# Performance work log

Measured on AMD Instinct MI355X. Metric: run time of the kernel, lower is better.

The kernel has to match this reference:

```python
import jax, jax.numpy as jnp
import numpy as np

B, DIM, S = 8, 512, 1024
H, DH = 8, 64
FF_INNER = 1024      # dim * (ff_mult//2)
CONV_INNER = 1024    # dim * expansion_factor
K = 31
PAD = (K - 1) // 2


def _bn(x, g, b):
    # eval-mode BatchNorm2d with running stats (0,1) absorbed: per-channel affine
    return x * g[None, :, None, None] + b[None, :, None, None]


def _pw(x, w, b):
    # 1x1 Conv2d == channel matmul. x: [B,C,S,1], w: [O,C]
    return jnp.einsum('oc,bcst->bost', w, x) + b[None, :, None, None]


def _ff(x, g, b, w1, b1, w2, b2):
    h = _pw(_bn(x, g, b), w1, b1)
    return _pw(jax.nn.silu(h), w2, b2)


def _attn(x, g, b, wq, bq, wk, bk, wv, bv, wo, bo):
    xn = _bn(x, g, b)
    q = _pw(xn, wq, bq)[..., 0].reshape(B, H, DH, S)
    k = _pw(xn, wk, bk)[..., 0].reshape(B, H, DH, S)
    v = _pw(xn, wv, bv)[..., 0].reshape(B, H, DH, S)
    scale = DH ** -0.5
    scores = jnp.einsum('bhds,bhdt->bhst', q, k) * scale   # [B,H,S,S]
    w = jax.nn.softmax(scores, axis=-1)
    o = jnp.einsum('bhst,bhdt->bhds', w, v).reshape(B, H * DH, S)[..., None]
    return _pw(o, wo, bo)


def _conv(x, g, b, pw1_w, pw1_b, dconv_w, dconv_b, cbn_g, cbn_b, pw2_w, pw2_b):
    h = _pw(_bn(x, g, b), pw1_w, pw1_b)          # [B,2*CONV_INNER,S,1]
    a, gate = jnp.split(h, 2, axis=1)
    h = a * jax.nn.sigmoid(gate)                  # GLU
    h = jnp.transpose(h, (0, 1, 3, 2))            # [B,C,1,S] so kernel (1,K) runs along seq
    h = jax.lax.conv_general_dilated(
        h, dconv_w, window_strides=(1, 1), padding=((0, 0), (PAD, PAD)),
        dimension_numbers=('NCHW', 'OIHW', 'NCHW'))
    h = jnp.transpose(h, (0, 1, 3, 2)) + dconv_b[None, :, None, None]
    h = jax.nn.silu(_bn(h, cbn_g, cbn_b))
    return _pw(h, pw2_w, pw2_b)


def setup_inputs() -> dict:
    key = jax.random.key(0)
    ks = iter(jax.random.split(key, 32))
    w = lambda *s: jax.random.normal(next(ks), s, jnp.float32) * 0.02
    d = {
        'x': jax.random.normal(next(ks), (B, DIM, S, 1), jnp.float32),
        'ff1_g': jnp.ones((DIM,)), 'ff1_b': jnp.zeros((DIM,)),
        'ff1_w1': w(FF_INNER, DIM), 'ff1_b1': jnp.zeros((FF_INNER,)),
        'ff1_w2': w(DIM, FF_INNER), 'ff1_b2': jnp.zeros((DIM,)),
        'attn_g': jnp.ones((DIM,)), 'attn_b': jnp.zeros((DIM,)),
        'wq': w(H * DH, DIM), 'bq': jnp.zeros((H * DH,)),
        'wk': w(H * DH, DIM), 'bk': jnp.zeros((H * DH,)),
        'wv': w(H * DH, DIM), 'bv': jnp.zeros((H * DH,)),
        'wo': w(DIM, H * DH), 'bo': jnp.zeros((DIM,)),
        'conv_g': jnp.ones((DIM,)), 'conv_b': jnp.zeros((DIM,)),
        'pw1_w': w(2 * CONV_INNER, DIM), 'pw1_b': jnp.zeros((2 * CONV_INNER,)),
        'dconv_w': w(CONV_INNER, CONV_INNER, 1, K), 'dconv_b': jnp.zeros((CONV_INNER,)),
        'cbn_g': jnp.ones((CONV_INNER,)), 'cbn_b': jnp.zeros((CONV_INNER,)),
        'pw2_w': w(DIM, CONV_INNER), 'pw2_b': jnp.zeros((DIM,)),
        'ff2_g': jnp.ones((DIM,)), 'ff2_b': jnp.zeros((DIM,)),
        'ff2_w1': w(FF_INNER, DIM), 'ff2_b1': jnp.zeros((FF_INNER,)),
        'ff2_w2': w(DIM, FF_INNER), 'ff2_b2': jnp.zeros((DIM,)),
        'fin_g': jnp.ones((DIM,)), 'fin_b': jnp.zeros((DIM,)),
    }
    return d


def reference(x, ff1_g, ff1_b, ff1_w1, ff1_b1, ff1_w2, ff1_b2,
              attn_g, attn_b, wq, bq, wk, bk, wv, bv, wo, bo,
              conv_g, conv_b, pw1_w, pw1_b, dconv_w, dconv_b, cbn_g, cbn_b, pw2_w, pw2_b,
              ff2_g, ff2_b, ff2_w1, ff2_b1, ff2_w2, ff2_b2, fin_g, fin_b):
    x1 = x + 0.5 * _ff(x, ff1_g, ff1_b, ff1_w1, ff1_b1, ff1_w2, ff1_b2)
    x2 = x1 + _attn(x1, attn_g, attn_b, wq, bq, wk, bk, wv, bv, wo, bo)
    x3 = x2 + _conv(x2, conv_g, conv_b, pw1_w, pw1_b, dconv_w, dconv_b, cbn_g, cbn_b, pw2_w, pw2_b)
    x4 = x3 + 0.5 * _ff(x3, ff2_g, ff2_b, ff2_w1, ff2_b1, ff2_w2, ff2_b2)
    return _bn(x4, fin_g, fin_b)
```

## Files before the change

kernel.cpp:

```cpp
#include <hip/hip_runtime.h>
#include <cstdint>
#include <cstddef>

using bf16 = __bf16;
typedef __bf16 bf16x8 __attribute__((ext_vector_type(8)));
typedef float f32x4 __attribute__((ext_vector_type(4)));
typedef unsigned int uint4v __attribute__((ext_vector_type(4)));

#define NB 8
#define DIM 512
#define SEQ 1024
#define NH 8
#define DH 64
#define CONV_INNER 1024
#define KW 31
#define PADW 15
#define HPRA 1056

__device__ __forceinline__ float fsigmoid(float x) { return 1.f / (1.f + __expf(-x)); }
__device__ __forceinline__ float fsilu(float x) { return x * fsigmoid(x); }

__device__ __forceinline__ void gld16(const bf16* g, bf16* l) {
  __builtin_amdgcn_global_load_lds(
      (const __attribute__((address_space(1))) unsigned int*)g,
      (__attribute__((address_space(3))) unsigned int*)l, 16, 0, 0);
}


__global__ __launch_bounds__(256) void k_diag(float* __restrict__ out, int n, float v) {
  int i = blockIdx.x * 256 + threadIdx.x;
  if (i < n) out[i] = v;
}


struct CvtArgs {
  const float* s[10];
  bf16* d[10];
  int cum[11];
};

__global__ __launch_bounds__(256) void k_convert_all(CvtArgs a) {
  int blk = blockIdx.x;
  int seg = 0;
#pragma unroll
  for (int t = 0; t < 10; ++t)
    if (blk >= a.cum[t + 1]) seg = t + 1;
  const float* src = a.s[seg];
  bf16* dst = a.d[seg];
  int i = ((blk - a.cum[seg]) * 256 + threadIdx.x) * 4;
  float4 v = *reinterpret_cast<const float4*>(src + i);
  dst[i]     = (bf16)v.x;
  dst[i + 1] = (bf16)v.y;
  dst[i + 2] = (bf16)v.z;
  dst[i + 3] = (bf16)v.w;
}

__global__ __launch_bounds__(256) void k_conv_wt(const float* __restrict__ w,
                                                 bf16* __restrict__ wt) {
  __shared__ float t[256 * KW];
  int o = blockIdx.x, i0 = blockIdx.y * 256;
  const float* src = w + (size_t)o * (CONV_INNER * KW) + (size_t)i0 * KW;
  for (int idx = threadIdx.x; idx < 256 * KW; idx += 256) t[idx] = src[idx];
  __syncthreads();
  for (int k = 0; k < KW; ++k) {
    wt[((size_t)k * CONV_INNER + o) * CONV_INNER + i0 + threadIdx.x] =
        (bf16)t[threadIdx.x * KW + k];
  }
}

__global__ __launch_bounds__(256) void k_pad_zero(bf16* __restrict__ hpad) {
  int i = blockIdx.x * 256 + threadIdx.x;
  int b = i / (32 * 128);
  int r = (i >> 7) & 31;
  int c8 = (i & 127) * 8;
  int row = (r < PADW) ? r : 1024 + r;
  uint4v z = {0u, 0u, 0u, 0u};
  *reinterpret_cast<uint4v*>(&hpad[((size_t)b * HPRA + row) * CONV_INNER + c8]) = z;
}

__global__ __launch_bounds__(256) void k_transpose_in(const float* __restrict__ x,
                                                      const float* __restrict__ g,
                                                      const float* __restrict__ bvec,
                                                      float* __restrict__ xT,
                                                      bf16* __restrict__ xbn) {
  __shared__ float t[32][33];
  int s0 = blockIdx.x * 32, c0 = blockIdx.y * 32, b = blockIdx.z;
  int col = threadIdx.x & 31, rq = threadIdx.x >> 5;
#pragma unroll
  for (int i = 0; i < 4; ++i) {
    int row = rq + i * 8;
    t[row][col] = x[((size_t)b * DIM + c0 + row) * SEQ + s0 + col];
  }
  __syncthreads();
  float gg = g[c0 + col], bb = bvec[c0 + col];
#pragma unroll
  for (int i = 0; i < 4; ++i) {
    int srow = rq + i * 8;
    float v = t[col][srow];
    size_t off = ((size_t)b * SEQ + s0 + srow) * DIM + c0 + col;
    xT[off] = v;
    xbn[off] = (bf16)(v * gg + bb);
  }
}

__global__ __launch_bounds__(256) void k_concat_bias(const float* __restrict__ bq,
                                                     const float* __restrict__ bk,
                                                     const float* __restrict__ bv,
                                                     float* __restrict__ qb) {
  int i = blockIdx.x * 256 + threadIdx.x;
  if (i < 512) qb[i] = bq[i];
  else if (i < 1024) qb[i] = bk[i - 512];
  else if (i < 1536) qb[i] = bv[i - 1024];
}

template <int EPI>
__global__ __launch_bounds__(256) void k_gemm(const bf16* __restrict__ A,
                                              const bf16* __restrict__ W,
                                              const float* __restrict__ bias,
                                              const float* __restrict__ res,
                                              const float* __restrict__ g,
                                              const float* __restrict__ bb,
                                              float* __restrict__ outf,
                                              bf16* __restrict__ outb, int N, int K) {
  __shared__ __align__(16) bf16 sA[2][128 * 64];
  __shared__ __align__(16) bf16 sB[2][128 * 64];
  const int tid = threadIdx.x;
  const int b = blockIdx.z;
  const int m0 = blockIdx.y * 128, n0 = blockIdx.x * 128;
  const int lane = tid & 63, wid = tid >> 6;
  const int wm = (wid & 1) * 64, wn = (wid >> 1) * 64;
  const int fr = lane & 15, fg = lane >> 4;
  const int srow = lane >> 3;
  const int scol = ((lane & 7) ^ srow) * 8;

  f32x4 acc[4][4];
#pragma unroll
  for (int i = 0; i < 4; ++i)
#pragma unroll
    for (int j = 0; j < 4; ++j) acc[i][j] = (f32x4)0.f;

  const bf16* Abase = A + ((size_t)b * SEQ + m0 + srow) * K + scol;
  const bf16* Wbase = W + (size_t)(n0 + srow) * K + scol;
  const int nch = K >> 6;

#pragma unroll
  for (int c = 0; c < 4; ++c) {
    const int ch = wid + c * 4;
    gld16(Abase + (size_t)(ch * 8) * K, &sA[0][ch * 512]);
    gld16(Wbase + (size_t)(ch * 8) * K, &sB[0][ch * 512]);
  }
  __syncthreads();

  int buf = 0;
  for (int kt = 0; kt < nch; ++kt) {
    if (kt + 1 < nch) {
      const int kc = (kt + 1) * 64;
#pragma unroll
      for (int c = 0; c < 4; ++c) {
        const int ch = wid + c * 4;
        gld16(Abase + (size_t)(ch * 8) * K + kc, &sA[buf ^ 1][ch * 512]);
        gld16(Wbase + (size_t)(ch * 8) * K + kc, &sB[buf ^ 1][ch * 512]);
      }
    }
#pragma unroll
    for (int kk = 0; kk < 2; ++kk) {
      const int cg = kk * 4 + fg;
      bf16x8 aF[4], bF[4];
#pragma unroll
      for (int i = 0; i < 4; ++i) {
        const int ar = wm + i * 16 + fr;
        aF[i] = *reinterpret_cast<const bf16x8*>(
            &sA[buf][ar * 64 + ((cg ^ (ar & 7)) * 8)]);
        const int br = wn + i * 16 + fr;
        bF[i] = *reinterpret_cast<const bf16x8*>(
            &sB[buf][br * 64 + ((cg ^ (br & 7)) * 8)]);
      }
#pragma unroll
      for (int mi = 0; mi < 4; ++mi)
#pragma unroll
        for (int ni = 0; ni < 4; ++ni)
          acc[mi][ni] = __builtin_amdgcn_mfma_f32_16x16x32_bf16(aF[mi], bF[ni],
                                                                acc[mi][ni], 0, 0, 0);
    }
    __syncthreads();
    buf ^= 1;
  }

#pragma unroll
  for (int mi = 0; mi < 4; ++mi) {
#pragma unroll
    for (int ni = 0; ni < 4; ++ni) {
      int ncol = n0 + wn + ni * 16 + fr;
      float bv = bias[ncol];
      if constexpr (EPI == 5) {
        float gg = g[ncol], bbv = bb[ncol];
        int mrow0 = m0 + wm + mi * 16 + fg * 4;
        float v[4];
#pragma unroll
        for (int j = 0; j < 4; ++j) {
          float a = acc[mi][ni][j] + bv;
          float r = res[((size_t)b * SEQ + mrow0 + j) * 512 + ncol] + 0.5f * a;
          v[j] = r * gg + bbv;
        }
        *reinterpret_cast<float4*>(outf + ((size_t)b * 512 + ncol) * SEQ + mrow0) =
            make_float4(v[0], v[1], v[2], v[3]);
      } else {
#pragma unroll
        for (int j = 0; j < 4; ++j) {
          int mrow = m0 + wm + mi * 16 + fg * 4 + j;
          size_t off = ((size_t)b * SEQ + mrow) * N + ncol;
          float a = acc[mi][ni][j] + bv;
          if constexpr (EPI == 0) {
            outb[off] = (bf16)fsilu(a);
          } else if constexpr (EPI == 2) {
            outb[off] = (bf16)a;
          } else if constexpr (EPI == 1) {
            float r = res[off] + 0.5f * a;
            outf[off] = r;
            outb[off] = (bf16)(r * g[ncol] + bb[ncol]);
          } else if constexpr (EPI == 3) {
            float r = res[off] + a;
            outf[off] = r;
            outb[off] = (bf16)(r * g[ncol] + bb[ncol]);
          }
        }
      }
    }
  }
}

__global__ __launch_bounds__(256) void k_pw1_glu(const bf16* __restrict__ A,
                                                 const bf16* __restrict__ W,
                                                 const float* __restrict__ bias,
                                                 bf16* __restrict__ hpad) {
  __shared__ __align__(16) bf16 sA[128 * 64];
  __shared__ __align__(16) bf16 sBa[128 * 64];
  __shared__ __align__(16) bf16 sBg[128 * 64];
  const int tid = threadIdx.x;
  const int b = blockIdx.z;
  const int m0 = blockIdx.y * 128, n0 = blockIdx.x * 128;
  const int lane = tid & 63, wid = tid >> 6;
  const int wm = (wid & 1) * 64, wn = (wid >> 1) * 64;
  const int fr = lane & 15, fg = lane >> 4;
  const int srow = lane >> 3;
  const int scol = ((lane & 7) ^ srow) * 8;
  const int K = 512;

  f32x4 accA[4][4], accG[4][4];
#pragma unroll
  for (int i = 0; i < 4; ++i)
#pragma unroll
    for (int j = 0; j < 4; ++j) { accA[i][j] = (f32x4)0.f; accG[i][j] = (f32x4)0.f; }

  const bf16* Abase = A + ((size_t)b * SEQ + m0 + srow) * K + scol;
  const bf16* WaB = W + (size_t)(n0 + srow) * K + scol;
  const bf16* WgB = W + (size_t)(n0 + 1024 + srow) * K + scol;

  for (int kt = 0; kt < 8; ++kt) {
    const int kc = kt * 64;
#pragma unroll
    for (int c = 0; c < 4; ++c) {
      const int ch = wid + c * 4;
      gld16(Abase + (size_t)(ch * 8) * K + kc, &sA[ch * 512]);
      gld16(WaB + (size_t)(ch * 8) * K + kc, &sBa[ch * 512]);
      gld16(WgB + (size_t)(ch * 8) * K + kc, &sBg[ch * 512]);
    }
    __syncthreads();
#pragma unroll
    for (int kk = 0; kk < 2; ++kk) {
      const int cg = kk * 4 + fg;
      bf16x8 aF[4], bFa[4], bFg[4];
#pragma unroll
      for (int i = 0; i < 4; ++i) {
        const int ar = wm + i * 16 + fr;
        aF[i] = *reinterpret_cast<const bf16x8*>(
            &sA[ar * 64 + ((cg ^ (ar & 7)) * 8)]);
        const int br = wn + i * 16 + fr;
        bFa[i] = *reinterpret_cast<const bf16x8*>(
            &sBa[br * 64 + ((cg ^ (br & 7)) * 8)]);
        bFg[i] = *reinterpret_cast<const bf16x8*>(
            &sBg[br * 64 + ((cg ^ (br & 7)) * 8)]);
      }
#pragma unroll
      for (int mi = 0; mi < 4; ++mi)
#pragma unroll
        for (int ni = 0; ni < 4; ++ni) {
          accA[mi][ni] =
              __builtin_amdgcn_mfma_f32_16x16x32_bf16(aF[mi], bFa[ni], accA[mi][ni], 0, 0, 0);
          accG[mi][ni] =
              __builtin_amdgcn_mfma_f32_16x16x32_bf16(aF[mi], bFg[ni], accG[mi][ni], 0, 0, 0);
        }
    }
    __syncthreads();
  }

#pragma unroll
  for (int mi = 0; mi < 4; ++mi) {
#pragma unroll
    for (int ni = 0; ni < 4; ++ni) {
      int ncol = n0 + wn + ni * 16 + fr;
      float ba = bias[ncol], bg = bias[ncol + 1024];
#pragma unroll
      for (int j = 0; j < 4; ++j) {
        int mrow = m0 + wm + mi * 16 + fg * 4 + j;
        float av = accA[mi][ni][j] + ba;
        float gv = accG[mi][ni][j] + bg;
        hpad[((size_t)b * HPRA + PADW + mrow) * CONV_INNER + ncol] =
            (bf16)(av * fsigmoid(gv));
      }
    }
  }
}

__global__ __launch_bounds__(256) void k_conv(const bf16* __restrict__ hpad,
                                              const bf16* __restrict__ wt,
                                              const float* __restrict__ bias,
                                              const float* __restrict__ g,
                                              const float* __restrict__ bb,
                                              bf16* __restrict__ outb) {
  __shared__ __align__(16) bf16 sA[160 * 64];
  __shared__ __align__(16) bf16 sB0[128 * 64];
  __shared__ __align__(16) bf16 sB1[128 * 64];
  const int tid = threadIdx.x;
  const int b = blockIdx.z;
  const int n0 = blockIdx.x * 128, m0 = blockIdx.y * 128;
  const int lane = tid & 63, wid = tid >> 6;
  const int wm = (wid & 1) * 64, wn = (wid >> 1) * 64;
  const int fr = lane & 15, fg = lane >> 4;
  const int srow = lane >> 3;
  const int scol = ((lane & 7) ^ srow) * 8;

  f32x4 acc[4][4];
#pragma unroll
  for (int i = 0; i < 4; ++i)
#pragma unroll
    for (int j = 0; j < 4; ++j) acc[i][j] = (f32x4)0.f;

  const bf16* Abase = hpad + ((size_t)b * HPRA + m0 + srow) * CONV_INNER + scol;
  const bf16* Wbase = wt + (size_t)(n0 + srow) * CONV_INNER + scol;

  for (int it = 0; it < 16; ++it) {
    const int itc = it * 64;
#pragma unroll
    for (int c = 0; c < 5; ++c) {
      const int ch = wid + c * 4;
      gld16(Abase + (size_t)(ch * 8) * CONV_INNER + itc, &sA[ch * 512]);
    }
#pragma unroll
    for (int c = 0; c < 4; ++c) {
      const int ch = wid + c * 4;
      gld16(Wbase + (size_t)(ch * 8) * CONV_INNER + itc, &sB0[ch * 512]);
    }
    __syncthreads();

    for (int ks = 0; ks < KW; ++ks) {
      const bf16* cur = (ks & 1) ? sB1 : sB0;
      bf16* nxt = (ks & 1) ? sB0 : sB1;
      if (ks + 1 < KW) {
#pragma unroll
        for (int c = 0; c < 4; ++c) {
          const int ch = wid + c * 4;
          gld16(Wbase + (size_t)(ks + 1) * CONV_INNER * CONV_INNER +
                    (size_t)(ch * 8) * CONV_INNER + itc,
                &nxt[ch * 512]);
        }
      }
#pragma unroll
      for (int kk = 0; kk < 2; ++kk) {
        const int cg = kk * 4 + fg;
        bf16x8 aF[4], bF[4];
#pragma unroll
        for (int i = 0; i < 4; ++i) {
          const int ar = ks + wm + i * 16 + fr;
          aF[i] = *reinterpret_cast<const bf16x8*>(
              &sA[ar * 64 + ((cg ^ (ar & 7)) * 8)]);
        }
#pragma unroll
        for (int n = 0; n < 4; ++n) {
          const int br = wn + n * 16 + fr;
          bF[n] = *reinterpret_cast<const bf16x8*>(
              &cur[br * 64 + ((cg ^ (br & 7)) * 8)]);
        }
#pragma unroll
        for (int mi = 0; mi < 4; ++mi)
#pragma unroll
          for (int ni = 0; ni < 4; ++ni)
            acc[mi][ni] = __builtin_amdgcn_mfma_f32_16x16x32_bf16(aF[mi], bF[ni],
                                                                  acc[mi][ni], 0, 0, 0);
      }
      __syncthreads();
    }
  }

#pragma unroll
  for (int mi = 0; mi < 4; ++mi) {
#pragma unroll
    for (int ni = 0; ni < 4; ++ni) {
      int ncol = n0 + wn + ni * 16 + fr;
      float bv = bias[ncol], gg = g[ncol], bbv = bb[ncol];
#pragma unroll
      for (int j = 0; j < 4; ++j) {
        int mrow = m0 + wm + mi * 16 + fg * 4 + j;
        float a = acc[mi][ni][j] + bv;
        outb[((size_t)b * SEQ + mrow) * CONV_INNER + ncol] = (bf16)fsilu(a * gg + bbv);
      }
    }
  }
}

__global__ __launch_bounds__(256) void k_attn(const bf16* __restrict__ qkv,
                                              bf16* __restrict__ out) {
  __shared__ __align__(16) bf16 sQ[128][72];
  __shared__ __align__(16) bf16 sK[64][72];
  __shared__ __align__(16) bf16 sVT[64][72];
  __shared__ __align__(16) bf16 sP[128][72];
  const int tid = threadIdx.x;
  const int bh = blockIdx.y;
  const int b = bh >> 3, h = bh & 7;
  const int m0 = blockIdx.x * 128;
  const int lane = tid & 63, wid = tid >> 6;
  const int w32 = wid * 32;
  const int fr = lane & 15, fg = lane >> 4;
  const size_t base = (size_t)b * SEQ * 1536;

  for (int idx = tid; idx < 128 * 8; idx += 256) {
    int row = idx >> 3, c = (idx & 7) * 8;
    *reinterpret_cast<uint4v*>(&sQ[row][c]) =
        *reinterpret_cast<const uint4v*>(qkv + base + (size_t)(m0 + row) * 1536 + h * 64 + c);
  }

  f32x4 o[2][4];
  float mst[2][4], lst[2][4];
#pragma unroll
  for (int mi = 0; mi < 2; ++mi)
#pragma unroll
    for (int j = 0; j < 4; ++j) {
      mst[mi][j] = -1e30f;
      lst[mi][j] = 0.f;
#pragma unroll
      for (int df = 0; df < 4; ++df) o[mi][df] = (f32x4)0.f;
    }

  for (int t0 = 0; t0 < SEQ; t0 += 64) {
    for (int idx = tid; idx < 64 * 8; idx += 256) {
      int row = idx >> 3, c = (idx & 7) * 8;
      *reinterpret_cast<uint4v*>(&sK[row][c]) = *reinterpret_cast<const uint4v*>(
          qkv + base + (size_t)(t0 + row) * 1536 + 512 + h * 64 + c);
    }
    for (int e = tid; e < 64 * 64; e += 256) {
      int t = e >> 6, d = e & 63;
      sVT[d][t] = qkv[base + (size_t)(t0 + t) * 1536 + 1024 + h * 64 + d];
    }
    __syncthreads();

    f32x4 sacc[2][4];
#pragma unroll
    for (int mi = 0; mi < 2; ++mi)
#pragma unroll
      for (int tf = 0; tf < 4; ++tf) sacc[mi][tf] = (f32x4)0.f;
#pragma unroll
    for (int kk = 0; kk < 2; ++kk) {
      bf16x8 aQ[2], bK[4];
#pragma unroll
      for (int mi = 0; mi < 2; ++mi)
        aQ[mi] = *reinterpret_cast<const bf16x8*>(&sQ[w32 + mi * 16 + fr][kk * 32 + fg * 8]);
#pragma unroll
      for (int tf = 0; tf < 4; ++tf)
        bK[tf] = *reinterpret_cast<const bf16x8*>(&sK[tf * 16 + fr][kk * 32 + fg * 8]);
#pragma unroll
      for (int mi = 0; mi < 2; ++mi)
#pragma unroll
        for (int tf = 0; tf < 4; ++tf)
          sacc[mi][tf] =
              __builtin_amdgcn_mfma_f32_16x16x32_bf16(aQ[mi], bK[tf], sacc[mi][tf], 0, 0, 0);
    }

#pragma unroll
    for (int mi = 0; mi < 2; ++mi) {
#pragma unroll
      for (int j = 0; j < 4; ++j) {
        float rm = -1e30f;
#pragma unroll
        for (int tf = 0; tf < 4; ++tf) rm = fmaxf(rm, sacc[mi][tf][j] * 0.125f);
#pragma unroll
        for (int off = 1; off < 16; off <<= 1) rm = fmaxf(rm, __shfl_xor(rm, off));
        float mnew = fmaxf(mst[mi][j], rm);
        float al = __expf(mst[mi][j] - mnew);
        float ps = 0.f;
#pragma unroll
        for (int tf = 0; tf < 4; ++tf) {
          float p = __expf(sacc[mi][tf][j] * 0.125f - mnew);
          ps += p;
          sP[w32 + mi * 16 + fg * 4 + j][tf * 16 + fr] = (bf16)p;
        }
#pragma unroll
        for (int off = 1; off < 16; off <<= 1) ps += __shfl_xor(ps, off);
        lst[mi][j] = lst[mi][j] * al + ps;
        mst[mi][j] = mnew;
#pragma unroll
        for (int df = 0; df < 4; ++df) o[mi][df][j] *= al;
      }
    }
    __syncthreads();

#pragma unroll
    for (int kk = 0; kk < 2; ++kk) {
      bf16x8 aP[2], bV[4];
#pragma unroll
      for (int mi = 0; mi < 2; ++mi)
        aP[mi] = *reinterpret_cast<const bf16x8*>(&sP[w32 + mi * 16 + fr][kk * 32 + fg * 8]);
#pragma unroll
      for (int df = 0; df < 4; ++df)
        bV[df] = *reinterpret_cast<const bf16x8*>(&sVT[df * 16 + fr][kk * 32 + fg * 8]);
#pragma unroll
      for (int mi = 0; mi < 2; ++mi)
#pragma unroll
        for (int df = 0; df < 4; ++df)
          o[mi][df] = __builtin_amdgcn_mfma_f32_16x16x32_bf16(aP[mi], bV[df], o[mi][df], 0, 0, 0);
    }
    __syncthreads();
  }

#pragma unroll
  for (int mi = 0; mi < 2; ++mi)
#pragma unroll
    for (int df = 0; df < 4; ++df)
#pragma unroll
      for (int j = 0; j < 4; ++j) {
        int row = m0 + w32 + mi * 16 + fg * 4 + j;
        int col = h * 64 + df * 16 + fr;
        out[((size_t)b * SEQ + row) * 512 + col] = (bf16)(o[mi][df][j] / lst[mi][j]);
      }
}


extern "C" void kernel_launch(void* const* d_in, const int* in_sizes, int n_in,
                              void* d_out, int out_size, void* d_ws, size_t ws_size,
                              hipStream_t stream) {
  const float* x      = (const float*)d_in[0];
  const float* ff1_g  = (const float*)d_in[1];
  const float* ff1_b  = (const float*)d_in[2];
  const float* ff1_w1 = (const float*)d_in[3];
  const float* ff1_b1 = (const float*)d_in[4];
  const float* ff1_w2 = (const float*)d_in[5];
  const float* ff1_b2 = (const float*)d_in[6];
  const float* attn_g = (const float*)d_in[7];
  const float* attn_b = (const float*)d_in[8];
  const float* wq     = (const float*)d_in[9];
  const float* bq     = (const float*)d_in[10];
  const float* wk     = (const float*)d_in[11];
  const float* bk     = (const float*)d_in[12];
  const float* wv     = (const float*)d_in[13];
  const float* bv     = (const float*)d_in[14];
  const float* wo     = (const float*)d_in[15];
  const float* bo     = (const float*)d_in[16];
  const float* conv_g = (const float*)d_in[17];
  const float* conv_b = (const float*)d_in[18];
  const float* pw1_w  = (const float*)d_in[19];
  const float* pw1_b  = (const float*)d_in[20];
  const float* dconv_w = (const float*)d_in[21];
  const float* dconv_b = (const float*)d_in[22];
  const float* cbn_g  = (const float*)d_in[23];
  const float* cbn_b  = (const float*)d_in[24];
  const float* pw2_w  = (const float*)d_in[25];
  const float* pw2_b  = (const float*)d_in[26];
  const float* ff2_g  = (const float*)d_in[27];
  const float* ff2_b  = (const float*)d_in[28];
  const float* ff2_w1 = (const float*)d_in[29];
  const float* ff2_b1 = (const float*)d_in[30];
  const float* ff2_w2 = (const float*)d_in[31];
  const float* ff2_b2 = (const float*)d_in[32];
  const float* fin_g  = (const float*)d_in[33];
  const float* fin_b  = (const float*)d_in[34];

  char* ws = (char*)d_ws;
  size_t off = 0;
  auto alloc = [&](size_t bytes) -> void* {
    off = (off + 255) & ~(size_t)255;
    void* p = ws + off;
    off += bytes;
    return p;
  };

  bf16* wqkv  = (bf16*)alloc((size_t)1536 * 512 * 2);
  float* qkvb = (float*)alloc(1536 * 4);
  bf16* wf1a  = (bf16*)alloc((size_t)1024 * 512 * 2);
  bf16* wf1b  = (bf16*)alloc((size_t)512 * 1024 * 2);
  bf16* wwo   = (bf16*)alloc((size_t)512 * 512 * 2);
  bf16* wpw1  = (bf16*)alloc((size_t)2048 * 512 * 2);
  bf16* wpw2  = (bf16*)alloc((size_t)512 * 1024 * 2);
  bf16* wf2a  = (bf16*)alloc((size_t)1024 * 512 * 2);
  bf16* wf2b  = (bf16*)alloc((size_t)512 * 1024 * 2);

  bf16*  Bn  = (bf16*)alloc((size_t)NB * SEQ * 512 * 2);
  float* F1  = (float*)alloc((size_t)NB * SEQ * 512 * 4);
  bf16*  HGp = (bf16*)alloc((size_t)NB * HPRA * 1024 * 2);
  bf16*  H2  = (bf16*)alloc((size_t)NB * SEQ * 1024 * 2);

  char* E = (char*)alloc((size_t)KW * 1024 * 1024 * 2);
  bf16*  wt     = (bf16*)E;
  bf16*  h1     = (bf16*)E;
  bf16*  qkv    = (bf16*)E;
  bf16*  attn_o = (bf16*)(E + (size_t)24 * 1024 * 1024);
  float* x1     = (float*)(E + (size_t)32 * 1024 * 1024);
  float* x3     = (float*)E;
  bf16*  h3     = (bf16*)(E + (size_t)16 * 1024 * 1024);

  float* xT = F1;
  float* x2 = F1;
  bf16* xbn = Bn, *x1bn = Bn, *x2bn = Bn, *x3bn = Bn;
  size_t needed = off;
  (void)in_sizes; (void)n_in;

  if (ws_size < needed) {
    k_diag<<<(out_size + 255) / 256, 256, 0, stream>>>(
        (float*)d_out, out_size, (float)(ws_size >> 20));
    return;
  }

  CvtArgs ca;
  ca.s[0] = wq;      ca.d[0] = wqkv;
  ca.s[1] = wk;      ca.d[1] = wqkv + 512 * 512;
  ca.s[2] = wv;      ca.d[2] = wqkv + 1024 * 512;
  ca.s[3] = ff1_w1;  ca.d[3] = wf1a;
  ca.s[4] = ff1_w2;  ca.d[4] = wf1b;
  ca.s[5] = wo;      ca.d[5] = wwo;
  ca.s[6] = pw1_w;   ca.d[6] = wpw1;
  ca.s[7] = pw2_w;   ca.d[7] = wpw2;
  ca.s[8] = ff2_w1;  ca.d[8] = wf2a;
  ca.s[9] = ff2_w2;  ca.d[9] = wf2b;
  int blocks1024[10] = {256, 256, 256, 512, 512, 256, 1024, 512, 512, 512};
  int cum = 0;
  for (int i = 0; i < 10; ++i) { ca.cum[i] = cum; cum += blocks1024[i]; }
  ca.cum[10] = cum;
  k_convert_all<<<cum, 256, 0, stream>>>(ca);
  k_concat_bias<<<6, 256, 0, stream>>>(bq, bk, bv, qkvb);
  k_pad_zero<<<(NB * 32 * 128) / 256, 256, 0, stream>>>(HGp);
  k_transpose_in<<<dim3(32, 16, NB), 256, 0, stream>>>(x, ff1_g, ff1_b, xT, xbn);

  k_gemm<0><<<dim3(8, 8, NB), 256, 0, stream>>>(xbn, wf1a, ff1_b1, nullptr, nullptr,
                                                nullptr, nullptr, h1, 1024, 512);
  k_gemm<1><<<dim3(4, 8, NB), 256, 0, stream>>>(h1, wf1b, ff1_b2, xT, attn_g, attn_b,
                                                x1, x1bn, 512, 1024);
  k_gemm<2><<<dim3(12, 8, NB), 256, 0, stream>>>(x1bn, wqkv, qkvb, nullptr, nullptr,
                                                 nullptr, nullptr, qkv, 1536, 512);
  k_attn<<<dim3(8, 64), 256, 0, stream>>>(qkv, attn_o);
  k_gemm<3><<<dim3(4, 8, NB), 256, 0, stream>>>(attn_o, wwo, bo, x1, conv_g, conv_b,
                                                x2, x2bn, 512, 512);
  k_conv_wt<<<dim3(1024, 4), 256, 0, stream>>>(dconv_w, wt);
  k_pw1_glu<<<dim3(8, 8, NB), 256, 0, stream>>>(x2bn, wpw1, pw1_b, HGp);
  k_conv<<<dim3(8, 8, NB), 256, 0, stream>>>(HGp, wt, dconv_b, cbn_g, cbn_b, H2);
  k_gemm<3><<<dim3(4, 8, NB), 256, 0, stream>>>(H2, wpw2, pw2_b, x2, ff2_g, ff2_b,
                                                x3, x3bn, 512, 1024);
  k_gemm<0><<<dim3(8, 8, NB), 256, 0, stream>>>(x3bn, wf2a, ff2_b1, nullptr, nullptr,
                                                nullptr, nullptr, h3, 1024, 512);
  k_gemm<5><<<dim3(4, 8, NB), 256, 0, stream>>>(h3, wf2b, ff2_b2, x3, fin_g, fin_b,
                                                (float*)d_out, nullptr, 512, 1024);
}
```

Measured before the change: 761.7 us.

## Write V transposed from QKV GEMM epilogue and vectorize conv weight transpose

The QKV projection GEMM gains an epilogue variant that writes the V part directly in a per-head [d][seq] layout into a separate buffer. The attention kernel can then fill its transposed-V shared tile with 16-byte vector loads instead of scalar strided gathers. Separately, the depthwise-conv weight transpose kernel now packs eight bf16 values per store instead of issuing scalar 2-byte stores. The cost is that the GEMM's V writes become strided scattered stores, plus an extra workspace region at a 48 MB offset that must not overlap live buffers.

```diff
diff --git a/kernel.cpp b/kernel.cpp
--- a/kernel.cpp
+++ b/kernel.cpp
@@ -62,9 +62,13 @@
   const float* src = w + (size_t)o * (CONV_INNER * KW) + (size_t)i0 * KW;
   for (int idx = threadIdx.x; idx < 256 * KW; idx += 256) t[idx] = src[idx];
   __syncthreads();
-  for (int k = 0; k < KW; ++k) {
-    wt[((size_t)k * CONV_INNER + o) * CONV_INNER + i0 + threadIdx.x] =
-        (bf16)t[threadIdx.x * KW + k];
+  for (int idx = threadIdx.x; idx < KW * 32; idx += 256) {
+    int k = idx >> 5, c = idx & 31;
+    bf16x8 v;
+#pragma unroll
+    for (int e = 0; e < 8; ++e) v[e] = (bf16)t[(c * 8 + e) * KW + k];
+    *reinterpret_cast<bf16x8*>(
+        &wt[((size_t)k * CONV_INNER + o) * CONV_INNER + i0 + c * 8]) = v;
   }
 }
 
@@ -121,7 +125,8 @@
                                               const float* __restrict__ g,
                                               const float* __restrict__ bb,
                                               float* __restrict__ outf,
-                                              bf16* __restrict__ outb, int N, int K) {
+                                              bf16* __restrict__ outb,
+                                              bf16* __restrict__ vtout, int N, int K) {
   __shared__ __align__(16) bf16 sA[2][128 * 64];
   __shared__ __align__(16) bf16 sB[2][128 * 64];
   const int tid = threadIdx.x;
@@ -214,6 +219,14 @@
             outb[off] = (bf16)fsilu(a);
           } else if constexpr (EPI == 2) {
             outb[off] = (bf16)a;
+          } else if constexpr (EPI == 6) {
+            if (ncol < 1024) {
+              outb[off] = (bf16)a;
+            } else {
+              int d = ncol - 1024;
+              vtout[(((size_t)b * 8 + (d >> 6)) * 64 + (d & 63)) * SEQ + mrow] =
+                  (bf16)a;
+            }
           } else if constexpr (EPI == 1) {
             float r = res[off] + 0.5f * a;
             outf[off] = r;
@@ -409,6 +422,7 @@
 }
 
 __global__ __launch_bounds__(256) void k_attn(const bf16* __restrict__ qkv,
+                                              const bf16* __restrict__ vT,
                                               bf16* __restrict__ out) {
   __shared__ __align__(16) bf16 sQ[128][72];
   __shared__ __align__(16) bf16 sK[64][72];
@@ -422,6 +436,7 @@
   const int w32 = wid * 32;
   const int fr = lane & 15, fg = lane >> 4;
   const size_t base = (size_t)b * SEQ * 1536;
+  const size_t vbase = (size_t)bh * 64 * SEQ;
 
   for (int idx = tid; idx < 128 * 8; idx += 256) {
     int row = idx >> 3, c = (idx & 7) * 8;
@@ -446,10 +461,8 @@
       int row = idx >> 3, c = (idx & 7) * 8;
       *reinterpret_cast<uint4v*>(&sK[row][c]) = *reinterpret_cast<const uint4v*>(
           qkv + base + (size_t)(t0 + row) * 1536 + 512 + h * 64 + c);
-    }
-    for (int e = tid; e < 64 * 64; e += 256) {
-      int t = e >> 6, d = e & 63;
-      sVT[d][t] = qkv[base + (size_t)(t0 + t) * 1536 + 1024 + h * 64 + d];
+      *reinterpret_cast<uint4v*>(&sVT[row][c]) = *reinterpret_cast<const uint4v*>(
+          vT + vbase + (size_t)row * SEQ + t0 + c);
     }
     __syncthreads();
 
@@ -603,6 +616,7 @@
   bf16*  qkv    = (bf16*)E;
   bf16*  attn_o = (bf16*)(E + (size_t)24 * 1024 * 1024);
   float* x1     = (float*)(E + (size_t)32 * 1024 * 1024);
+  bf16*  vT     = (bf16*)(E + (size_t)48 * 1024 * 1024);
   float* x3     = (float*)E;
   bf16*  h3     = (bf16*)(E + (size_t)16 * 1024 * 1024);
 
@@ -639,21 +653,21 @@
   k_transpose_in<<<dim3(32, 16, NB), 256, 0, stream>>>(x, ff1_g, ff1_b, xT, xbn);
 
   k_gemm<0><<<dim3(8, 8, NB), 256, 0, stream>>>(xbn, wf1a, ff1_b1, nullptr, nullptr,
-                                                nullptr, nullptr, h1, 1024, 512);
+                                                nullptr, nullptr, h1, nullptr, 1024, 512);
   k_gemm<1><<<dim3(4, 8, NB), 256, 0, stream>>>(h1, wf1b, ff1_b2, xT, attn_g, attn_b,
-                                                x1, x1bn, 512, 1024);
-  k_gemm<2><<<dim3(12, 8, NB), 256, 0, stream>>>(x1bn, wqkv, qkvb, nullptr, nullptr,
-                                                 nullptr, nullptr, qkv, 1536, 512);
-  k_attn<<<dim3(8, 64), 256, 0, stream>>>(qkv, attn_o);
+                                                x1, x1bn, nullptr, 512, 1024);
+  k_gemm<6><<<dim3(12, 8, NB), 256, 0, stream>>>(x1bn, wqkv, qkvb, nullptr, nullptr,
+                                                 nullptr, nullptr, qkv, vT, 1536, 512);
+  k_attn<<<dim3(8, 64), 256, 0, stream>>>(qkv, vT, attn_o);
   k_gemm<3><<<dim3(4, 8, NB), 256, 0, stream>>>(attn_o, wwo, bo, x1, conv_g, conv_b,
-                                                x2, x2bn, 512, 512);
+                                                x2, x2bn, nullptr, 512, 512);
   k_conv_wt<<<dim3(1024, 4), 256, 0, stream>>>(dconv_w, wt);
   k_pw1_glu<<<dim3(8, 8, NB), 256, 0, stream>>>(x2bn, wpw1, pw1_b, HGp);
   k_conv<<<dim3(8, 8, NB), 256, 0, stream>>>(HGp, wt, dconv_b, cbn_g, cbn_b, H2);
   k_gemm<3><<<dim3(4, 8, NB), 256, 0, stream>>>(H2, wpw2, pw2_b, x2, ff2_g, ff2_b,
-                                                x3, x3bn, 512, 1024);
+                                                x3, x3bn, nullptr, 512, 1024);
   k_gemm<0><<<dim3(8, 8, NB), 256, 0, stream>>>(x3bn, wf2a, ff2_b1, nullptr, nullptr,
-                                                nullptr, nullptr, h3, 1024, 512);
+                                                nullptr, nullptr, h3, nullptr, 1024, 512);
   k_gemm<5><<<dim3(4, 8, NB), 256, 0, stream>>>(h3, wf2b, ff2_b2, x3, fin_g, fin_b,
-                                                (float*)d_out, nullptr, 512, 1024);
-}
+                                                (float*)d_out, nullptr, nullptr, 512, 1024);
+}
```

New measurement: 761.7 us. No clear change (+0.0%).
